# Performance work log

Measured on AMD Instinct MI355X. Metric: run time of the kernel, lower is better.

The kernel has to match this reference:

```python
import jax, jax.numpy as jnp
import numpy as np

N = 50000
E = 800000
IN_DIM = 128
HID = 32
HEADS = 8
OUT_DIM = 64
OUT_CLASSES = 2
NEG_SLOPE = 0.01  # torch F.leaky_relu default


def _leaky(x):
    return jax.nn.leaky_relu(x, NEG_SLOPE)


def _seg_softmax(logits, seg, n):
    # softmax over edges grouped by destination node (DGL mailbox softmax)
    m = jax.ops.segment_max(logits, seg, num_segments=n)
    m = jnp.where(jnp.isfinite(m), m, 0.0)  # empty segments -> -inf guard
    ex = jnp.exp(logits - m[seg])
    den = jax.ops.segment_sum(ex, seg, num_segments=n)
    return ex / jnp.maximum(den[seg], 1e-12)


def _gat_layer(h, gate, src, dst, fc, a_src, a_dst):
    # fc: [H, in, out]; a_src/a_dst: [H, out] (split of attn_fc weight over the concat)
    n = h.shape[0]
    z = jnp.einsum('ni,hio->nho', h, fc)            # [N,H,O]
    zs = z[src]                                      # [E,H,O] gather over edges
    e = _leaky(jnp.einsum('eho,ho->eh', zs, a_src)
               + jnp.einsum('eho,ho->eh', z[dst], a_dst))  # [E,H]
    alpha = _seg_softmax(e * gate, dst, n)           # gate: [E,1] broadcast
    out = jax.ops.segment_sum(alpha[..., None] * zs, dst, num_segments=n)  # [N,H,O]
    return out.reshape(n, -1)                        # head concat


def setup_inputs() -> dict:
    key = jax.random.key(0)
    ks = jax.random.split(key, 16)
    h = jax.random.normal(ks[0], (N, IN_DIM), dtype=jnp.float32)
    src = jax.random.randint(ks[1], (E,), 0, N)
    dst = jax.random.randint(ks[2], (E,), 0, N)
    def lin(k, fan_in, shape):
        return jax.random.normal(k, shape, dtype=jnp.float32) / np.sqrt(fan_in)
    return {
        'h': h, 'src': src, 'dst': dst,
        # MLPPredictor (gate): W1 in->16, W2 32->8, W3 8->1
        'W1': lin(ks[3], IN_DIM, (IN_DIM, 16)), 'b1': jnp.zeros((16,), jnp.float32),
        'W2': lin(ks[4], 32, (32, 8)),          'b2': jnp.zeros((8,), jnp.float32),
        'W3': lin(ks[5], 8, (8, 1)),            'b3': jnp.zeros((1,), jnp.float32),
        # layer1: HEADS independent GateGATLayers (stacked)
        'fc1': lin(ks[6], IN_DIM, (HEADS, IN_DIM, HID)),
        'a1_src': lin(ks[7], 2 * HID, (HEADS, HID)),
        'a1_dst': lin(ks[8], 2 * HID, (HEADS, HID)),
        # layer2: single head, in = HEADS*HID -> OUT_DIM
        'fc2': lin(ks[9], HEADS * HID, (1, HEADS * HID, OUT_DIM)),
        'a2_src': lin(ks[10], 2 * OUT_DIM, (1, OUT_DIM)),
        'a2_dst': lin(ks[11], 2 * OUT_DIM, (1, OUT_DIM)),
        # MLPEdgePredictor: 2*OUT_DIM -> OUT_CLASSES
        'Wp': lin(ks[12], 2 * OUT_DIM, (2 * OUT_DIM, OUT_CLASSES)),
        'bp': jnp.zeros((OUT_CLASSES,), jnp.float32),
    }


def reference(h, src, dst, W1, b1, W2, b2, W3, b3,
              fc1, a1_src, a1_dst, fc2, a2_src, a2_dst, Wp, bp):
    # --- layer0: MLPPredictor gate (detached + min-max normalized in original) ---
    h1 = h @ W1 + b1                                   # [N,16]
    cat = jnp.concatenate([h1[src], h1[dst]], axis=1)  # [E,32]
    s = jnp.maximum(cat @ W2 + b2, 0.0) @ W3 + b3      # [E,1]
    gate = (s - s.min()) / (s.max() - s.min())         # [E,1] in [0,1]
    gate = jax.lax.stop_gradient(gate)                 # original detaches to numpy
    # --- layer1: multi-head gated GAT, leaky_relu, then single-head layer ---
    hA = _leaky(_gat_layer(h, gate, src, dst, fc1, a1_src, a1_dst))   # [N, HEADS*HID]
    hB = _gat_layer(hA, gate, src, dst, fc2, a2_src, a2_dst)          # [N, OUT_DIM]
    # --- MLPEdgePredictor ---
    edge_score = jnp.concatenate([hB[src], hB[dst]], axis=1) @ Wp + bp  # [E, OUT_CLASSES]
    return edge_score, gate
```

## Files before the change

### kernel.cpp

```cpp
#include <hip/hip_runtime.h>
#include <math.h>

#define FINF __builtin_inff()

using short8  = __attribute__((ext_vector_type(8))) short;
using floatx4 = __attribute__((ext_vector_type(4))) float;
union U4 { uint4 u; short8 s; };

__device__ __forceinline__ float leaky(float x){ return x > 0.f ? x : 0.01f*x; }

__device__ __forceinline__ unsigned int f2bf(float f){
  unsigned int x = __float_as_uint(f);
  x += 0x7FFFu + ((x >> 16) & 1u);
  return x >> 16;
}
__device__ __forceinline__ unsigned int pack2(float lo, float hi){
  return f2bf(lo) | (f2bf(hi) << 16);
}
__device__ __forceinline__ float bflo(unsigned int u){ return __uint_as_float(u << 16); }
__device__ __forceinline__ float bfhi(unsigned int u){ return __uint_as_float(u & 0xFFFF0000u); }

__global__ __launch_bounds__(256) void k_prep(const float* __restrict__ fc1,
        const float* __restrict__ fc2, const float* __restrict__ W1,
        const float* __restrict__ W2, const float* __restrict__ b1,
        const float* __restrict__ a1s, const float* __restrict__ a1d,
        const float* __restrict__ a2s, const float* __restrict__ a2d,
        unsigned short* __restrict__ wp1, unsigned short* __restrict__ wp2,
        float* __restrict__ ubias, int* __restrict__ counts8, int N){
  int b = blockIdx.x, t = threadIdx.x;
  if (b < 224){
    int idx = b*256 + t;
    if (idx < 32768){
      int i  = idx & 7;
      int l  = (idx >> 3) & 63;
      int kk = (idx >> 9) & 3;
      int nt = idx >> 11;
      int n = nt*16 + (l & 15);
      int k = kk*32 + ((l >> 4) << 3) + i;
      wp1[idx] = (unsigned short)f2bf(fc1[(size_t)(n >> 5)*4096 + k*32 + (n & 31)]);
    } else if (idx < 34816){
      int j = idx - 32768;
      int i = j & 7, l = (j >> 3) & 63, kk = j >> 9;
      int k = kk*32 + ((l >> 4) << 3) + i;
      int c = l & 15, hh = c >> 1;
      const float* f = fc1 + (size_t)hh*4096 + (size_t)k*32;
      const float* av = (c & 1) ? (a1d + hh*32) : (a1s + hh*32);
      float s = 0.f;
      #pragma unroll
      for (int o = 0; o < 32; o++) s += f[o]*av[o];
      wp1[idx] = (unsigned short)f2bf(s);
    } else if (idx < 36864){
      int j = idx - 34816;
      int i = j & 7, l = (j >> 3) & 63, kk = j >> 9;
      int k = kk*32 + ((l >> 4) << 3) + i;
      int c = l & 15;
      float s = 0.f;
      if (c < 8){
        #pragma unroll
        for (int o = 0; o < 16; o++) s += W1[k*16 + o]*W2[o*8 + c];
      } else {
        #pragma unroll
        for (int o = 0; o < 16; o++) s += W1[k*16 + o]*W2[(16 + o)*8 + (c - 8)];
      }
      wp1[idx] = (unsigned short)f2bf(s);
    } else {
      int j = idx - 36864;
      if (j < 16384){
        int i  = j & 7, l = (j >> 3) & 63, kk = (j >> 9) & 7, nt = j >> 12;
        int n = nt*16 + (l & 15);
        int k = kk*32 + ((l >> 4) << 3) + i;
        wp2[j] = (unsigned short)f2bf(fc2[(size_t)k*64 + n]);
      } else {
        int q = j - 16384;
        int i = q & 7, l = (q >> 3) & 63, kk = q >> 9;
        int k = kk*32 + ((l >> 4) << 3) + i;
        int c = l & 15;
        float s = 0.f;
        if (c == 0){
          for (int o = 0; o < 64; o++) s += fc2[(size_t)k*64 + o]*a2s[o];
        } else if (c == 1){
          for (int o = 0; o < 64; o++) s += fc2[(size_t)k*64 + o]*a2d[o];
        }
        wp2[j] = (unsigned short)f2bf(s);
      }
    }
  } else if (b == 224){
    if (t < 16){
      float s = 0.f;
      if (t < 8){
        #pragma unroll
        for (int o = 0; o < 16; o++) s += b1[o]*W2[o*8 + t];
      } else {
        #pragma unroll
        for (int o = 0; o < 16; o++) s += b1[o]*W2[(16 + o)*8 + (t - 8)];
      }
      ubias[t] = s;
    }
  } else {
    int i = (b - 225)*256 + t;
    if (i < N*8) counts8[i] = 0;
  }
}

__global__ __launch_bounds__(256) void k_z1m(const float* __restrict__ h,
        const unsigned short* __restrict__ wp1, const float* __restrict__ ubias,
        unsigned short* __restrict__ z1u, float* __restrict__ es1,
        float* __restrict__ ed1, float* __restrict__ u_s, float* __restrict__ u_d,
        int N){
  __shared__ uint4 lw[4096];
  int t = threadIdx.x;
  const uint4* wp4 = (const uint4*)wp1;
  #pragma unroll
  for (int i = 0; i < 16; i++) lw[t + i*256] = wp4[t + i*256];
  __syncthreads();
  int l = t & 63, wv = t >> 6;
  int n0 = blockIdx.x*64, m0 = wv*16;
  int rowA = min(n0 + m0 + (l & 15), N-1);
  const float* hr = h + (size_t)rowA*128 + ((l >> 4) << 3);
  U4 a[4];
  #pragma unroll
  for (int kk = 0; kk < 4; kk++){
    float4 f0 = *(const float4*)(hr + kk*32);
    float4 f1 = *(const float4*)(hr + kk*32 + 4);
    a[kk].u.x = pack2(f0.x, f0.y); a[kk].u.y = pack2(f0.z, f0.w);
    a[kk].u.z = pack2(f1.x, f1.y); a[kk].u.w = pack2(f1.z, f1.w);
  }
  int node0 = n0 + m0 + ((l >> 4) << 2);
  int c = l & 15;
  float ub = ubias[c];
  #pragma unroll
  for (int nt = 0; nt < 18; nt++){
    floatx4 acc;
    float b0 = (nt == 17) ? ub : 0.f;
    acc[0] = b0; acc[1] = b0; acc[2] = b0; acc[3] = b0;
    #pragma unroll
    for (int kk = 0; kk < 4; kk++){
      U4 bfr;
      bfr.u = (nt < 16) ? lw[(nt*4 + kk)*64 + l] : wp4[(nt*4 + kk)*64 + l];
      acc = __builtin_amdgcn_mfma_f32_16x16x32_bf16(a[kk].s, bfr.s, acc, 0, 0, 0);
    }
    if (nt < 16){
      int col = nt*16 + c;
      #pragma unroll
      for (int i2 = 0; i2 < 4; i2++){
        int node = node0 + i2;
        if (node < N) z1u[(size_t)node*256 + col] = (unsigned short)f2bf(acc[i2]);
      }
    } else if (nt == 16){
      int hh = c >> 1;
      #pragma unroll
      for (int i2 = 0; i2 < 4; i2++){
        int node = node0 + i2;
        if (node < N){
          if (c & 1) ed1[node*8 + hh] = acc[i2];
          else       es1[node*8 + hh] = acc[i2];
        }
      }
    } else {
      #pragma unroll
      for (int i2 = 0; i2 < 4; i2++){
        int node = node0 + i2;
        if (node < N){
          if (c < 8) u_s[(size_t)node*8 + c] = acc[i2];
          else       u_d[(size_t)node*8 + (c - 8)] = acc[i2];
        }
      }
    }
  }
}

__global__ __launch_bounds__(256) void k_gate_edge(const float* __restrict__ u_s,
        const float* __restrict__ u_d,
        const int* __restrict__ src, const int* __restrict__ dst,
        const float* __restrict__ b2, const float* __restrict__ W3,
        const float* __restrict__ b3,
        float* __restrict__ sbuf, int* __restrict__ counts8,
        int* __restrict__ rank, float2* __restrict__ pmm, int E, int N){
  __shared__ float lb2[8], lw3[8];
  __shared__ float lb3;
  __shared__ float rmin[4], rmax[4];
  int t = threadIdx.x;
  if (t < 8){ lb2[t] = b2[t]; lw3[t] = W3[t]; }
  if (t == 8) lb3 = b3[0];
  __syncthreads();
  int e = blockIdx.x*blockDim.x + t;
  float s = 0.f;
  bool valid = (e < E);
  if (valid){
    int a = src[e], b = dst[e];
    float4 us0 = ((const float4*)(u_s + (size_t)a*8))[0];
    float4 us1 = ((const float4*)(u_s + (size_t)a*8))[1];
    float4 ud0 = ((const float4*)(u_d + (size_t)b*8))[0];
    float4 ud1 = ((const float4*)(u_d + (size_t)b*8))[1];
    float tv[8] = { us0.x+ud0.x, us0.y+ud0.y, us0.z+ud0.z, us0.w+ud0.w,
                    us1.x+ud1.x, us1.y+ud1.y, us1.z+ud1.z, us1.w+ud1.w };
    s = lb3;
    #pragma unroll
    for (int j = 0; j < 8; j++) s += fmaxf(tv[j] + lb2[j], 0.f)*lw3[j];
    sbuf[e] = s;
    rank[e] = atomicAdd(&counts8[(size_t)(blockIdx.x & 7)*N + b], 1);
  }
  float vmin = valid ? s : FINF;
  float vmax = valid ? s : -FINF;
  #pragma unroll
  for (int o = 32; o > 0; o >>= 1){
    vmin = fminf(vmin, __shfl_xor(vmin, o));
    vmax = fmaxf(vmax, __shfl_xor(vmax, o));
  }
  if ((t & 63) == 0){ rmin[t >> 6] = vmin; rmax[t >> 6] = vmax; }
  __syncthreads();
  if (t == 0){
    float mn = fminf(fminf(rmin[0], rmin[1]), fminf(rmin[2], rmin[3]));
    float mx = fmaxf(fmaxf(rmax[0], rmax[1]), fmaxf(rmax[2], rmax[3]));
    pmm[blockIdx.x] = make_float2(mn, mx);
  }
}

__global__ __launch_bounds__(256) void k_scan1(const int* __restrict__ counts8,
        int* __restrict__ indptr, int* __restrict__ blockSums, int N){
  __shared__ int wsum[4];
  int t = threadIdx.x;
  int base = blockIdx.x*1024 + t*4;
  int c[4];
  #pragma unroll
  for (int i = 0; i < 4; i++) c[i] = 0;
  for (int r = 0; r < 8; r++){
    const int* cr = counts8 + (size_t)r*N;
    #pragma unroll
    for (int i = 0; i < 4; i++) if (base + i < N) c[i] += cr[base + i];
  }
  int s = c[0] + c[1] + c[2] + c[3];
  int lane = t & 63, wid = t >> 6;
  int inc = s;
  #pragma unroll
  for (int o = 1; o < 64; o <<= 1){
    int v = __shfl_up(inc, o);
    if (lane >= o) inc += v;
  }
  if (lane == 63) wsum[wid] = inc;
  __syncthreads();
  int woff = 0;
  #pragma unroll
  for (int i = 0; i < 4; i++) if (i < wid) woff += wsum[i];
  int run = woff + inc - s;
  #pragma unroll
  for (int i = 0; i < 4; i++){
    if (base + i < N) indptr[base + i] = run;
    run += c[i];
  }
  if (t == 255) blockSums[blockIdx.x] = woff + inc;
}

__global__ __launch_bounds__(64) void k_scan2(int* __restrict__ blockSums,
        int* __restrict__ indptr, int B, int N,
        const float2* __restrict__ pmm, int GB, float* __restrict__ minmax){
  int t = threadIdx.x;
  int carry = 0;
  for (int b0 = 0; b0 < B; b0 += 64){
    int idx = b0 + t;
    int v = (idx < B) ? blockSums[idx] : 0;
    int inc = v;
    #pragma unroll
    for (int o = 1; o < 64; o <<= 1){
      int u = __shfl_up(inc, o);
      if (t >= o) inc += u;
    }
    if (idx < B) blockSums[idx] = carry + inc - v;
    carry += __shfl(inc, 63);
  }
  if (t == 0) indptr[N] = carry;
  float mn = FINF, mx = -FINF;
  for (int i = t; i < GB; i += 64){
    float2 v = pmm[i];
    mn = fminf(mn, v.x);
    mx = fmaxf(mx, v.y);
  }
  #pragma unroll
  for (int o = 32; o > 0; o >>= 1){
    mn = fminf(mn, __shfl_xor(mn, o));
    mx = fmaxf(mx, __shfl_xor(mx, o));
  }
  if (t == 0){ minmax[0] = mn; minmax[1] = mx; }
}

__global__ __launch_bounds__(256) void k_scan3(int* __restrict__ indptr,
        const int* __restrict__ blockSums, const int* __restrict__ counts8,
        int* __restrict__ repoff, int N){
  int i = blockIdx.x*blockDim.x + threadIdx.x;
  if (i >= N) return;
  int v = indptr[i] + blockSums[i >> 10];
  indptr[i] = v;
  int run = v;
  for (int r = 0; r < 8; r++){
    repoff[(size_t)r*N + i] = run;
    run += counts8[(size_t)r*N + i];
  }
}

__global__ void k_scatter(const int* __restrict__ src, const int* __restrict__ dst,
                          const float* __restrict__ sbuf, const float* __restrict__ minmax,
                          const int* __restrict__ rank, const int* __restrict__ repoff,
                          float* __restrict__ gate_out, uint2* __restrict__ eg,
                          int E, int N){
  int e = blockIdx.x*blockDim.x + threadIdx.x;
  if (e >= E) return;
  float mn = minmax[0], mx = minmax[1];
  float g = (sbuf[e] - mn) / (mx - mn);
  gate_out[e] = g;
  int r = blockIdx.x & 7;
  int pos = repoff[(size_t)r*N + dst[e]] + rank[e];
  uint2 v; v.x = (unsigned int)src[e]; v.y = __float_as_uint(g);
  eg[pos] = v;
}

__global__ __launch_bounds__(256) void k_gather1f(const int* __restrict__ indptr,
        const uint2* __restrict__ eg, const float* __restrict__ es1,
        const float* __restrict__ ed1, const unsigned int* __restrict__ z1b,
        unsigned int* __restrict__ hAb, int N){
  __shared__ float lap[4][64][8];
  int t = threadIdx.x;
  int w = t >> 6, lane = t & 63;
  int n = blockIdx.x*4 + w;
  if (n >= N) return;
  int hh = lane >> 3;
  float4 ev0 = *(const float4*)(ed1 + (size_t)n*8);
  float4 ev1 = *(const float4*)(ed1 + (size_t)n*8 + 4);
  int beg = indptr[n], end = indptr[n+1];
  float4 acc = make_float4(0.f,0.f,0.f,0.f);
  float den = 0.f;
  for (int c = beg; c < end; c += 64){
    int len = min(64, end - c);
    int sv = 0;
    if (lane < len){
      uint2 v = eg[c + lane];
      sv = (int)v.x;
      float g = __uint_as_float(v.y);
      float4 e0 = *(const float4*)(es1 + (size_t)sv*8);
      float4 e1 = *(const float4*)(es1 + (size_t)sv*8 + 4);
      float4 w0, w1;
      w0.x = __expf(leaky(e0.x + ev0.x)*g);
      w0.y = __expf(leaky(e0.y + ev0.y)*g);
      w0.z = __expf(leaky(e0.z + ev0.z)*g);
      w0.w = __expf(leaky(e0.w + ev0.w)*g);
      w1.x = __expf(leaky(e1.x + ev1.x)*g);
      w1.y = __expf(leaky(e1.y + ev1.y)*g);
      w1.z = __expf(leaky(e1.z + ev1.z)*g);
      w1.w = __expf(leaky(e1.w + ev1.w)*g);
      *(float4*)&lap[w][lane][0] = w0;
      *(float4*)&lap[w][lane][4] = w1;
    }
    __builtin_amdgcn_wave_barrier();
    for (int jj = 0; jj < len; jj++){
      int a = __shfl(sv, jj);
      float wgt = lap[w][jj][hh];
      uint2 zv = *(const uint2*)(z1b + (size_t)a*128 + lane*2);
      den += wgt;
      acc.x += wgt*bflo(zv.x); acc.y += wgt*bfhi(zv.x);
      acc.z += wgt*bflo(zv.y); acc.w += wgt*bfhi(zv.y);
    }
    __builtin_amdgcn_wave_barrier();
  }
  float iv = 1.f / fmaxf(den, 1e-12f);
  uint2 o;
  o.x = pack2(leaky(acc.x*iv), leaky(acc.y*iv));
  o.y = pack2(leaky(acc.z*iv), leaky(acc.w*iv));
  *(uint2*)(hAb + (size_t)n*128 + lane*2) = o;
}

__global__ __launch_bounds__(256) void k_z2m(const unsigned short* __restrict__ hAu,
        const unsigned short* __restrict__ wp2, unsigned short* __restrict__ z2u,
        float* __restrict__ es2, float* __restrict__ ed2, int N){
  __shared__ uint4 lw[2048];
  int t = threadIdx.x;
  const uint4* wp4 = (const uint4*)wp2;
  #pragma unroll
  for (int i = 0; i < 8; i++) lw[t + i*256] = wp4[t + i*256];
  __syncthreads();
  int l = t & 63, wv = t >> 6;
  int n0 = blockIdx.x*64, m0 = wv*16;
  int rowA = min(n0 + m0 + (l & 15), N-1);
  const unsigned short* ar = hAu + (size_t)rowA*256 + ((l >> 4) << 3);
  U4 a[8];
  #pragma unroll
  for (int kk = 0; kk < 8; kk++)
    a[kk].u = *(const uint4*)(ar + kk*32);
  int node0 = n0 + m0 + ((l >> 4) << 2);
  int c = l & 15;
  #pragma unroll
  for (int nt = 0; nt < 5; nt++){
    floatx4 acc = {0.f, 0.f, 0.f, 0.f};
    #pragma unroll
    for (int kk = 0; kk < 8; kk++){
      U4 bfr;
      bfr.u = (nt < 4) ? lw[(nt*8 + kk)*64 + l] : wp4[(nt*8 + kk)*64 + l];
      acc = __builtin_amdgcn_mfma_f32_16x16x32_bf16(a[kk].s, bfr.s, acc, 0, 0, 0);
    }
    if (nt < 4){
      int col = nt*16 + c;
      #pragma unroll
      for (int i2 = 0; i2 < 4; i2++){
        int node = node0 + i2;
        if (node < N) z2u[(size_t)node*64 + col] = (unsigned short)f2bf(acc[i2]);
      }
    } else {
      #pragma unroll
      for (int i2 = 0; i2 < 4; i2++){
        int node = node0 + i2;
        if (node < N){
          if (c == 0) es2[node] = acc[i2];
          else if (c == 1) ed2[node] = acc[i2];
        }
      }
    }
  }
}

__global__ __launch_bounds__(256) void k_gather2f(const int* __restrict__ indptr,
        const uint2* __restrict__ eg, const float* __restrict__ es2,
        const float* __restrict__ ed2, const unsigned int* __restrict__ z2b,
        const float* __restrict__ Wp, float* __restrict__ ps, float* __restrict__ pd,
        int N){
  __shared__ float lwp[256];
  int t = threadIdx.x;
  lwp[t] = Wp[t];
  __syncthreads();
  int n = blockIdx.x*8 + (t >> 5);
  if (n >= N) return;
  int l = t & 31;
  int sb = t & 32;
  float ed = ed2[n];
  int beg = indptr[n], end = indptr[n+1];
  float a0 = 0.f, a1 = 0.f, den = 0.f;
  for (int c = beg; c < end; c += 32){
    int len = min(32, end - c);
    int sv = 0; float wr = 0.f;
    if (l < len){
      uint2 v = eg[c + l];
      sv = (int)v.x;
      wr = __expf(leaky(es2[sv] + ed) * __uint_as_float(v.y));
    }
    for (int jj = 0; jj < len; jj++){
      int a = __shfl(sv, sb + jj);
      float wgt = __shfl(wr, sb + jj);
      unsigned int u = z2b[(size_t)a*32 + l];
      den += wgt;
      a0 += wgt*bflo(u);
      a1 += wgt*bfhi(u);
    }
  }
  float iv = 1.f / fmaxf(den, 1e-12f);
  float h0 = a0*iv, h1 = a1*iv;
  float s0 = h0*lwp[4*l+0] + h1*lwp[4*l+2];
  float s1 = h0*lwp[4*l+1] + h1*lwp[4*l+3];
  float d0 = h0*lwp[128+4*l+0] + h1*lwp[128+4*l+2];
  float d1 = h0*lwp[128+4*l+1] + h1*lwp[128+4*l+3];
  #pragma unroll
  for (int o = 1; o < 32; o <<= 1){
    s0 += __shfl_xor(s0, o); s1 += __shfl_xor(s1, o);
    d0 += __shfl_xor(d0, o); d1 += __shfl_xor(d1, o);
  }
  if (l == 0){
    ps[(size_t)n*2]   = s0; ps[(size_t)n*2+1] = s1;
    pd[(size_t)n*2]   = d0; pd[(size_t)n*2+1] = d1;
  }
}

__global__ void k_edgepred(const int* __restrict__ src, const int* __restrict__ dst,
                           const float* __restrict__ ps, const float* __restrict__ pd,
                           const float* __restrict__ bp, float* __restrict__ out, int E){
  int e = blockIdx.x*blockDim.x + threadIdx.x;
  if (e >= E) return;
  int a = src[e], b = dst[e];
  float2 vs = ((const float2*)ps)[a];
  float2 vd = ((const float2*)pd)[b];
  float2 o;
  o.x = vs.x + vd.x + bp[0];
  o.y = vs.y + vd.y + bp[1];
  ((float2*)out)[e] = o;
}

extern "C" void kernel_launch(void* const* d_in, const int* in_sizes, int n_in,
                              void* d_out, int out_size, void* d_ws, size_t ws_size,
                              hipStream_t stream) {
  const float* h   = (const float*)d_in[0];
  const int*   src = (const int*)d_in[1];
  const int*   dst = (const int*)d_in[2];
  const float* W1  = (const float*)d_in[3];
  const float* b1  = (const float*)d_in[4];
  const float* W2  = (const float*)d_in[5];
  const float* b2  = (const float*)d_in[6];
  const float* W3  = (const float*)d_in[7];
  const float* b3  = (const float*)d_in[8];
  const float* fc1 = (const float*)d_in[9];
  const float* a1s = (const float*)d_in[10];
  const float* a1d = (const float*)d_in[11];
  const float* fc2 = (const float*)d_in[12];
  const float* a2s = (const float*)d_in[13];
  const float* a2d = (const float*)d_in[14];
  const float* Wp  = (const float*)d_in[15];
  const float* bp  = (const float*)d_in[16];

  const int N = in_sizes[0] / 128;
  const int E = in_sizes[1];

  float* out_score = (float*)d_out;
  float* gate      = out_score + (size_t)E*2;

  char* w = (char*)d_ws;
  size_t off = 0;
  auto alloc = [&](size_t bytes) -> void* {
    off = (off + 255) & ~(size_t)255;
    void* p = w + off; off += bytes; return p;
  };
  float* u_s  = (float*)alloc((size_t)N*8*4);
  float* u_d  = (float*)alloc((size_t)N*8*4);
  unsigned short* z1u = (unsigned short*)alloc((size_t)N*256*2);
  float* es1  = (float*)alloc((size_t)N*8*4);
  float* ed1  = (float*)alloc((size_t)N*8*4);
  float* sbuf = (float*)alloc((size_t)E*4);
  unsigned short* hAu = (unsigned short*)alloc((size_t)N*256*2);
  float* es2  = (float*)alloc((size_t)N*4);
  float* ed2  = (float*)alloc((size_t)N*4);
  float* minmax = (float*)alloc(2*4);
  float* ubias  = (float*)alloc(16*4);
  int* counts8 = (int*)alloc((size_t)N*8*4);
  int* repoff  = (int*)alloc((size_t)N*8*4);
  int* rank    = (int*)alloc((size_t)E*4);
  int* indptr = (int*)alloc(((size_t)N+1)*4);
  int* blockSums = (int*)alloc(1024*4);
  const int GATE_B = (E + 255)/256;
  float2* pmm = (float2*)alloc((size_t)GATE_B*8);
  uint2* eg   = (uint2*)alloc((size_t)E*8);
  unsigned short* wp1 = (unsigned short*)alloc(36864*2);
  unsigned short* wp2 = (unsigned short*)alloc(20480*2);
  (void)ws_size; (void)n_in; (void)out_size;

  unsigned short* z2u = z1u;
  float* ps  = u_s;
  float* pd  = u_d;

  const int SCAN_B = (N + 1023)/1024;
  const int INIT_B = (N*8 + 255)/256;

  k_prep<<<225 + INIT_B, 256, 0, stream>>>(fc1, fc2, W1, W2, b1, a1s, a1d,
                                           a2s, a2d, wp1, wp2, ubias, counts8, N);
  k_z1m<<<(N + 63)/64, 256, 0, stream>>>(h, wp1, ubias, z1u, es1, ed1, u_s, u_d, N);
  k_gate_edge<<<GATE_B, 256, 0, stream>>>(u_s, u_d, src, dst, b2, W3, b3,
                                          sbuf, counts8, rank, pmm, E, N);
  k_scan1<<<SCAN_B, 256, 0, stream>>>(counts8, indptr, blockSums, N);
  k_scan2<<<1, 64, 0, stream>>>(blockSums, indptr, SCAN_B, N, pmm, GATE_B, minmax);
  k_scan3<<<(N + 255)/256, 256, 0, stream>>>(indptr, blockSums, counts8, repoff, N);
  k_scatter<<<GATE_B, 256, 0, stream>>>(src, dst, sbuf, minmax, rank, repoff,
                                        gate, eg, E, N);
  k_gather1f<<<(N + 3)/4, 256, 0, stream>>>(indptr, eg, es1, ed1,
                                            (const unsigned int*)z1u,
                                            (unsigned int*)hAu, N);
  k_z2m<<<(N + 63)/64, 256, 0, stream>>>(hAu, wp2, z2u, es2, ed2, N);
  k_gather2f<<<(N + 7)/8, 256, 0, stream>>>(indptr, eg, es2, ed2,
                                            (const unsigned int*)z2u,
                                            Wp, ps, pd, N);
  k_edgepred<<<(E + 255)/256, 256, 0, stream>>>(src, dst, ps, pd, bp, out_score, E);
}
```

Baseline: 228.7 us.

## Fuse layer-1 gather aggregation with layer-2 projection MFMA in one kernel

Merges the layer-1 neighbour aggregation kernel with the layer-2 linear projection. Each block aggregates 16 destination nodes into a shared-memory tile of hA, then runs the bf16 MFMA projection straight from LDS, with the output tiles spread across waves. This removes the hA round trip through global memory and one kernel launch. In exchange, each wave now handles 4 nodes serially, the block synchronises between the two phases, and the weight tiles are read from global memory instead of being staged in LDS. z2u gets its own buffer because z1u is still being read during the fused kernel.

```diff
diff --git a/kernel.cpp b/kernel.cpp
--- a/kernel.cpp
+++ b/kernel.cpp
@@ -313,86 +313,79 @@
   eg[pos] = v;
 }
 
-__global__ __launch_bounds__(256) void k_gather1f(const int* __restrict__ indptr,
+__global__ __launch_bounds__(256) void k_gather1z(const int* __restrict__ indptr,
         const uint2* __restrict__ eg, const float* __restrict__ es1,
         const float* __restrict__ ed1, const unsigned int* __restrict__ z1b,
-        unsigned int* __restrict__ hAb, int N){
+        const unsigned short* __restrict__ wp2, unsigned short* __restrict__ z2u,
+        float* __restrict__ es2, float* __restrict__ ed2, int N){
   __shared__ float lap[4][64][8];
+  __shared__ unsigned short lha[16*264];
   int t = threadIdx.x;
   int w = t >> 6, lane = t & 63;
-  int n = blockIdx.x*4 + w;
-  if (n >= N) return;
   int hh = lane >> 3;
-  float4 ev0 = *(const float4*)(ed1 + (size_t)n*8);
-  float4 ev1 = *(const float4*)(ed1 + (size_t)n*8 + 4);
-  int beg = indptr[n], end = indptr[n+1];
-  float4 acc = make_float4(0.f,0.f,0.f,0.f);
-  float den = 0.f;
-  for (int c = beg; c < end; c += 64){
-    int len = min(64, end - c);
-    int sv = 0;
-    if (lane < len){
-      uint2 v = eg[c + lane];
-      sv = (int)v.x;
-      float g = __uint_as_float(v.y);
-      float4 e0 = *(const float4*)(es1 + (size_t)sv*8);
-      float4 e1 = *(const float4*)(es1 + (size_t)sv*8 + 4);
-      float4 w0, w1;
-      w0.x = __expf(leaky(e0.x + ev0.x)*g);
-      w0.y = __expf(leaky(e0.y + ev0.y)*g);
-      w0.z = __expf(leaky(e0.z + ev0.z)*g);
-      w0.w = __expf(leaky(e0.w + ev0.w)*g);
-      w1.x = __expf(leaky(e1.x + ev1.x)*g);
-      w1.y = __expf(leaky(e1.y + ev1.y)*g);
-      w1.z = __expf(leaky(e1.z + ev1.z)*g);
-      w1.w = __expf(leaky(e1.w + ev1.w)*g);
-      *(float4*)&lap[w][lane][0] = w0;
-      *(float4*)&lap[w][lane][4] = w1;
-    }
-    __builtin_amdgcn_wave_barrier();
-    for (int jj = 0; jj < len; jj++){
-      int a = __shfl(sv, jj);
-      float wgt = lap[w][jj][hh];
-      uint2 zv = *(const uint2*)(z1b + (size_t)a*128 + lane*2);
-      den += wgt;
-      acc.x += wgt*bflo(zv.x); acc.y += wgt*bfhi(zv.x);
-      acc.z += wgt*bflo(zv.y); acc.w += wgt*bfhi(zv.y);
-    }
-    __builtin_amdgcn_wave_barrier();
-  }
-  float iv = 1.f / fmaxf(den, 1e-12f);
-  uint2 o;
-  o.x = pack2(leaky(acc.x*iv), leaky(acc.y*iv));
-  o.y = pack2(leaky(acc.z*iv), leaky(acc.w*iv));
-  *(uint2*)(hAb + (size_t)n*128 + lane*2) = o;
-}
-
-__global__ __launch_bounds__(256) void k_z2m(const unsigned short* __restrict__ hAu,
-        const unsigned short* __restrict__ wp2, unsigned short* __restrict__ z2u,
-        float* __restrict__ es2, float* __restrict__ ed2, int N){
-  __shared__ uint4 lw[2048];
-  int t = threadIdx.x;
+  int nb = blockIdx.x*16;
+  for (int j = 0; j < 4; j++){
+    int row = w*4 + j;
+    int n = nb + row;
+    uint2 orow = make_uint2(0u, 0u);
+    if (n < N){
+      float4 ev0 = *(const float4*)(ed1 + (size_t)n*8);
+      float4 ev1 = *(const float4*)(ed1 + (size_t)n*8 + 4);
+      int beg = indptr[n], end = indptr[n+1];
+      float4 acc = make_float4(0.f,0.f,0.f,0.f);
+      float den = 0.f;
+      for (int c = beg; c < end; c += 64){
+        int len = min(64, end - c);
+        int sv = 0;
+        if (lane < len){
+          uint2 v = eg[c + lane];
+          sv = (int)v.x;
+          float g = __uint_as_float(v.y);
+          float4 e0 = *(const float4*)(es1 + (size_t)sv*8);
+          float4 e1 = *(const float4*)(es1 + (size_t)sv*8 + 4);
+          float4 w0, w1;
+          w0.x = __expf(leaky(e0.x + ev0.x)*g);
+          w0.y = __expf(leaky(e0.y + ev0.y)*g);
+          w0.z = __expf(leaky(e0.z + ev0.z)*g);
+          w0.w = __expf(leaky(e0.w + ev0.w)*g);
+          w1.x = __expf(leaky(e1.x + ev1.x)*g);
+          w1.y = __expf(leaky(e1.y + ev1.y)*g);
+          w1.z = __expf(leaky(e1.z + ev1.z)*g);
+          w1.w = __expf(leaky(e1.w + ev1.w)*g);
+          *(float4*)&lap[w][lane][0] = w0;
+          *(float4*)&lap[w][lane][4] = w1;
+        }
+        __builtin_amdgcn_wave_barrier();
+        for (int jj = 0; jj < len; jj++){
+          int a = __shfl(sv, jj);
+          float wgt = lap[w][jj][hh];
+          uint2 zv = *(const uint2*)(z1b + (size_t)a*128 + lane*2);
+          den += wgt;
+          acc.x += wgt*bflo(zv.x); acc.y += wgt*bfhi(zv.x);
+          acc.z += wgt*bflo(zv.y); acc.w += wgt*bfhi(zv.y);
+        }
+        __builtin_amdgcn_wave_barrier();
+      }
+      float iv = 1.f / fmaxf(den, 1e-12f);
+      orow.x = pack2(leaky(acc.x*iv), leaky(acc.y*iv));
+      orow.y = pack2(leaky(acc.z*iv), leaky(acc.w*iv));
+    }
+    *(uint2*)(lha + row*264 + lane*4) = orow;
+  }
+  __syncthreads();
   const uint4* wp4 = (const uint4*)wp2;
-  #pragma unroll
-  for (int i = 0; i < 8; i++) lw[t + i*256] = wp4[t + i*256];
-  __syncthreads();
-  int l = t & 63, wv = t >> 6;
-  int n0 = blockIdx.x*64, m0 = wv*16;
-  int rowA = min(n0 + m0 + (l & 15), N-1);
-  const unsigned short* ar = hAu + (size_t)rowA*256 + ((l >> 4) << 3);
+  int arow = lane & 15, aoff = (lane >> 4)*8;
   U4 a[8];
   #pragma unroll
   for (int kk = 0; kk < 8; kk++)
-    a[kk].u = *(const uint4*)(ar + kk*32);
-  int node0 = n0 + m0 + ((l >> 4) << 2);
-  int c = l & 15;
-  #pragma unroll
-  for (int nt = 0; nt < 5; nt++){
+    a[kk].u = *(const uint4*)(lha + arow*264 + kk*32 + aoff);
+  int node0 = nb + ((lane >> 4) << 2);
+  int c = lane & 15;
+  for (int nt = w; nt < 5; nt += 4){
     floatx4 acc = {0.f, 0.f, 0.f, 0.f};
     #pragma unroll
     for (int kk = 0; kk < 8; kk++){
-      U4 bfr;
-      bfr.u = (nt < 4) ? lw[(nt*8 + kk)*64 + l] : wp4[(nt*8 + kk)*64 + l];
+      U4 bfr; bfr.u = wp4[(nt*8 + kk)*64 + lane];
       acc = __builtin_amdgcn_mfma_f32_16x16x32_bf16(a[kk].s, bfr.s, acc, 0, 0, 0);
     }
     if (nt < 4){
@@ -515,10 +508,10 @@
   float* u_s  = (float*)alloc((size_t)N*8*4);
   float* u_d  = (float*)alloc((size_t)N*8*4);
   unsigned short* z1u = (unsigned short*)alloc((size_t)N*256*2);
+  unsigned short* z2u = (unsigned short*)alloc((size_t)N*64*2);
   float* es1  = (float*)alloc((size_t)N*8*4);
   float* ed1  = (float*)alloc((size_t)N*8*4);
   float* sbuf = (float*)alloc((size_t)E*4);
-  unsigned short* hAu = (unsigned short*)alloc((size_t)N*256*2);
   float* es2  = (float*)alloc((size_t)N*4);
   float* ed2  = (float*)alloc((size_t)N*4);
   float* minmax = (float*)alloc(2*4);
@@ -535,7 +528,6 @@
   unsigned short* wp2 = (unsigned short*)alloc(20480*2);
   (void)ws_size; (void)n_in; (void)out_size;
 
-  unsigned short* z2u = z1u;
   float* ps  = u_s;
   float* pd  = u_d;
 
@@ -552,10 +544,9 @@
   k_scan3<<<(N + 255)/256, 256, 0, stream>>>(indptr, blockSums, counts8, repoff, N);
   k_scatter<<<GATE_B, 256, 0, stream>>>(src, dst, sbuf, minmax, rank, repoff,
                                         gate, eg, E, N);
-  k_gather1f<<<(N + 3)/4, 256, 0, stream>>>(indptr, eg, es1, ed1,
-                                            (const unsigned int*)z1u,
-                                            (unsigned int*)hAu, N);
-  k_z2m<<<(N + 63)/64, 256, 0, stream>>>(hAu, wp2, z2u, es2, ed2, N);
+  k_gather1z<<<(N + 15)/16, 256, 0, stream>>>(indptr, eg, es1, ed1,
+                                              (const unsigned int*)z1u,
+                                              wp2, z2u, es2, ed2, N);
   k_gather2f<<<(N + 7)/8, 256, 0, stream>>>(indptr, eg, es2, ed2,
                                             (const unsigned int*)z2u,
                                             Wp, ps, pd, N);
```

Measured after the change: 229.2 us. No clear change (+0.2%).
